# Optimization experiments

Measured on AMD Instinct MI355X. Metric: run time of the kernel, lower is better.

Reference implementation:

```python
import jax, jax.numpy as jnp
import numpy as np

C0 = 32          # cs[0] == cs[1] with planes=[32,32,...], cr=1.0
CIN = 4
EPS = 1e-5

# ---------- host-side coordinate hashing (mirrors F.sphash / F.sphashquery) ----------

def _enc(c):
    # unique int64 code per (x,y,z); +2 shift keeps offset-adjusted coords positive
    return (c[:, 0] + 2).astype(np.int64) + (c[:, 1] + 2).astype(np.int64) * 1024 \
        + (c[:, 2] + 2).astype(np.int64) * 1024 * 1024

def _lookup(sorted_codes, q):
    pos = np.searchsorted(sorted_codes, q)
    pos = np.minimum(pos, len(sorted_codes) - 1)
    return np.where(sorted_codes[pos] == q, pos, -1).astype(np.int32)

def _offsets(r):
    return np.array([[i, j, k] for i in r for j in r for k in r], np.int64)


def setup_inputs() -> dict:
    rng = np.random.default_rng(0)
    N0 = 400000
    pts = rng.integers(0, [400, 400, 40], size=(600000, 3)).astype(np.int64)
    codes = _enc(pts)
    codes_u, idx = np.unique(codes, return_index=True)
    assert len(codes_u) >= N0
    coords0, codes0 = pts[idx][:N0], codes_u[:N0]   # sorted by hash code

    off27, off8 = _offsets([-1, 0, 1]), _offsets([0, 1])
    # ks=3 stride=1 kernel map at level 0: nbr0[k, i] = index of coords0[i]+off27[k] (or -1)
    nbr0 = np.stack([_lookup(codes0, _enc(coords0 + o)) for o in off27])

    # stride-2 downsample coords (level 1)
    c1all = coords0 // 2
    codes1_u, i1 = np.unique(_enc(c1all), return_index=True)
    coords1 = c1all[i1]
    # ks=2 stride=2 kernel map: output voxel gathers inputs at 2*out + {0,1}^3
    down1 = np.stack([_lookup(codes0, _enc(coords1 * 2 + o)) for o in off8])
    # ks=3 stride=1 kernel map at level 1
    nbr1 = np.stack([_lookup(codes1_u, _enc(coords1 + o)) for o in off27])

    key = jax.random.key(0)
    ks = jax.random.split(key, 10)

    def w(k, K, ci, co):
        return jax.random.normal(k, (K, ci, co), jnp.float32) * (1.0 / np.sqrt(K * ci))

    return {
        "voxel_features": jax.random.normal(ks[0], (N0, CIN), jnp.float32),
        "W_stem1": w(ks[1], 27, CIN, C0),
        "W_stem2": w(ks[2], 27, C0, C0),
        "W_down":  w(ks[3], 8,  C0, C0),
        "W_r1a":   w(ks[4], 27, C0, C0),
        "W_r1b":   w(ks[5], 27, C0, C0),
        "W_r2a":   w(ks[6], 27, C0, C0),
        "W_r2b":   w(ks[7], 27, C0, C0),
        "gammas": jnp.ones((7, C0), jnp.float32),
        "betas":  jnp.zeros((7, C0), jnp.float32),
        "nbr0":  jnp.asarray(nbr0),
        "down1": jnp.asarray(down1),
        "nbr1":  jnp.asarray(nbr1),
    }


# ---------- sparse conv: gather-GEMM-scatter per kernel offset ----------

def _spconv(feat, nbr, W):
    # feat [N, Ci], nbr [K, M] (-1 = no neighbor), W [K, Ci, Co] -> out [M, Co]
    def step(acc, kw):
        idx, Wk = kw
        g = jnp.where((idx >= 0)[:, None], feat[jnp.maximum(idx, 0)], 0.0)
        return acc + g @ Wk, None
    acc0 = jnp.zeros((nbr.shape[1], W.shape[-1]), feat.dtype)
    out, _ = jax.lax.scan(step, acc0, (nbr, W))
    return out


def _bn(x, g, b):
    # BatchNorm1d, training-mode statistics (biased var), gamma/beta affine
    mu = x.mean(0)
    var = x.var(0)
    return (x - mu) * jax.lax.rsqrt(var + EPS) * g + b


def _cbr(x, nbr, W, g, b):
    return jax.nn.relu(_bn(_spconv(x, nbr, W), g, b))


def reference(voxel_features, W_stem1, W_stem2, W_down, W_r1a, W_r1b, W_r2a, W_r2b,
              gammas, betas, nbr0, down1, nbr1):
    g, b = gammas, betas
    # stem: two ks=3 sparse convs + BN + ReLU at level 0
    x = _cbr(voxel_features, nbr0, W_stem1, g[0], b[0])
    x = _cbr(x, nbr0, W_stem2, g[1], b[1])
    # stage1: BasicConvolutionBlock (ks=2, stride=2) + 2 ResidualBlocks at level 1
    x1 = _cbr(x, down1, W_down, g[2], b[2])
    h = _cbr(x1, nbr1, W_r1a, g[3], b[3])
    h = _bn(_spconv(h, nbr1, W_r1b), g[4], b[4])
    x1 = jax.nn.relu(h + x1)          # downsample == Identity (inc == outc, stride 1)
    h = _cbr(x1, nbr1, W_r2a, g[5], b[5])
    h = _bn(_spconv(h, nbr1, W_r2b), g[6], b[6])
    return jax.nn.relu(h + x1)
```

## Files before the change

kernel.cpp:

```cpp
#include <hip/hip_runtime.h>

#define EPS 1e-5f

typedef __attribute__((ext_vector_type(8))) short short8;
typedef __attribute__((ext_vector_type(4))) float floatx4;
typedef __attribute__((ext_vector_type(8))) unsigned short ushort8;
typedef __attribute__((ext_vector_type(4))) unsigned short ushortv4;

__device__ __forceinline__ unsigned short f2bf(float f) {
    union { float f; unsigned u; } x; x.f = f;
    unsigned r = x.u + 0x7fffu + ((x.u >> 16) & 1u);
    return (unsigned short)(r >> 16);
}
__device__ __forceinline__ float bf2f(unsigned short b) {
    union { unsigned u; float f; } x; x.u = ((unsigned)b) << 16;
    return x.f;
}

__global__ __launch_bounds__(256) void cvt_kernel(
    const float* __restrict__ x, unsigned short* __restrict__ o, int N)
{
    int t = blockIdx.x * 256 + threadIdx.x;
    if (t >= N) return;
    float4 v = *(const float4*)(x + (size_t)t * 4);
    ushortv4 r = {f2bf(v.x), f2bf(v.y), f2bf(v.z), f2bf(v.w)};
    *(ushortv4*)(o + (size_t)t * 4) = r;
}

__global__ __launch_bounds__(256) void pack_w_kernel(
    const float* __restrict__ W, unsigned short* __restrict__ out, int K)
{
    int t = blockIdx.x * 256 + threadIdx.x;
    if (t >= K * 128) return;
    int lane = t & 63;
    int h = (t >> 6) & 1;
    int k = t >> 7;
    int m = lane & 15, q = lane >> 4;
    ushort8 v;
#pragma unroll
    for (int j = 0; j < 8; ++j)
        v[j] = f2bf(W[((size_t)k * 32 + q * 8 + j) * 32 + h * 16 + m]);
    *(ushort8*)(out + (size_t)t * 8) = v;
}

__global__ __launch_bounds__(256) void pack_w1_kernel(
    const float* __restrict__ W, unsigned short* __restrict__ out)
{
    int t = blockIdx.x * 256 + threadIdx.x;
    if (t >= 512) return;
    int lane = t & 63;
    int h = (t >> 6) & 1;
    int c = t >> 7;
    int m = lane & 15, q = lane >> 4;
    ushort8 v;
#pragma unroll
    for (int j = 0; j < 8; ++j) {
        int kdim = c * 32 + q * 8 + j;
        int tap = kdim >> 2, ci = kdim & 3;
        v[j] = (tap < 27) ? f2bf(W[((size_t)tap * 4 + ci) * 32 + h * 16 + m]) : 0;
    }
    *(ushort8*)(out + (size_t)t * 8) = v;
}

__device__ __forceinline__ void conv_epilogue(
    floatx4 acc00, floatx4 acc01, floatx4 acc10, floatx4 acc11,
    unsigned short* __restrict__ y, float* __restrict__ part,
    int rowbase, int N, float* sm)
{
    const int lane = threadIdx.x & 63;
    const int m = lane & 15, q = lane >> 4;

    if (threadIdx.x < 64) sm[threadIdx.x] = 0.f;
    __syncthreads();

#pragma unroll
    for (int r = 0; r < 4; ++r) {
        int ra = rowbase + q * 4 + r;
        int rb = ra + 16;
        if (ra < N) {
            y[(size_t)ra * 32 + m]      = f2bf(acc00[r]);
            y[(size_t)ra * 32 + 16 + m] = f2bf(acc01[r]);
        }
        if (rb < N) {
            y[(size_t)rb * 32 + m]      = f2bf(acc10[r]);
            y[(size_t)rb * 32 + 16 + m] = f2bf(acc11[r]);
        }
    }

    float s0 = 0.f, q0 = 0.f, s1 = 0.f, q1 = 0.f;
#pragma unroll
    for (int r = 0; r < 4; ++r) {
        s0 += acc00[r] + acc10[r];
        q0 += acc00[r] * acc00[r] + acc10[r] * acc10[r];
        s1 += acc01[r] + acc11[r];
        q1 += acc01[r] * acc01[r] + acc11[r] * acc11[r];
    }
    s0 += __shfl_down(s0, 32); s0 += __shfl_down(s0, 16);
    q0 += __shfl_down(q0, 32); q0 += __shfl_down(q0, 16);
    s1 += __shfl_down(s1, 32); s1 += __shfl_down(s1, 16);
    q1 += __shfl_down(q1, 32); q1 += __shfl_down(q1, 16);
    if (lane < 16) {
        atomicAdd(&sm[m],      s0);
        atomicAdd(&sm[32 + m], q0);
        atomicAdd(&sm[16 + m],      s1);
        atomicAdd(&sm[48 + m], q1);
    }
    __syncthreads();
    if (threadIdx.x < 64)
        part[(size_t)blockIdx.x * 64 + threadIdx.x] = sm[threadIdx.x];
}

template <int K>
__global__ __launch_bounds__(256) void conv_mfma_kernel(
    const unsigned short* __restrict__ x,
    const int* __restrict__ nbr,
    const unsigned short* __restrict__ Wp,
    unsigned short* __restrict__ y,
    float* __restrict__ part, int N)
{
    __shared__ float sm[64];
    const int lane = threadIdx.x & 63;
    const int wave = threadIdx.x >> 6;
    const int m = lane & 15, q = lane >> 4;
    const int rowbase = blockIdx.x * 128 + wave * 32;
    const int row0 = rowbase + m;
    const int row1 = rowbase + 16 + m;

    floatx4 acc00 = {0.f, 0.f, 0.f, 0.f};
    floatx4 acc01 = acc00, acc10 = acc00, acc11 = acc00;

    for (int k = 0; k < K; ++k) {
        int i0 = (row0 < N) ? nbr[(size_t)k * N + row0] : -1;
        int i1 = (row1 < N) ? nbr[(size_t)k * N + row1] : -1;
        short8 a0 = {}, a1 = {};
        if (i0 >= 0) a0 = *(const short8*)(x + (size_t)i0 * 32 + q * 8);
        if (i1 >= 0) a1 = *(const short8*)(x + (size_t)i1 * 32 + q * 8);
        const short8* wk = (const short8*)(Wp + (size_t)k * 2 * 64 * 8);
        short8 b0 = wk[lane];
        short8 b1 = wk[64 + lane];
        acc00 = __builtin_amdgcn_mfma_f32_16x16x32_bf16(a0, b0, acc00, 0, 0, 0);
        acc01 = __builtin_amdgcn_mfma_f32_16x16x32_bf16(a0, b1, acc01, 0, 0, 0);
        acc10 = __builtin_amdgcn_mfma_f32_16x16x32_bf16(a1, b0, acc10, 0, 0, 0);
        acc11 = __builtin_amdgcn_mfma_f32_16x16x32_bf16(a1, b1, acc11, 0, 0, 0);
    }

    conv_epilogue(acc00, acc01, acc10, acc11, y, part, rowbase, N, sm);
}

__global__ __launch_bounds__(256) void conv_stem1_mfma(
    const unsigned short* __restrict__ xb,
    const int* __restrict__ nbr,
    const unsigned short* __restrict__ Wp,
    unsigned short* __restrict__ y,
    float* __restrict__ part, int N)
{
    __shared__ float sm[64];
    const int lane = threadIdx.x & 63;
    const int wave = threadIdx.x >> 6;
    const int m = lane & 15, q = lane >> 4;
    const int rowbase = blockIdx.x * 128 + wave * 32;
    const int row0 = rowbase + m;
    const int row1 = rowbase + 16 + m;

    floatx4 acc00 = {0.f, 0.f, 0.f, 0.f};
    floatx4 acc01 = acc00, acc10 = acc00, acc11 = acc00;

#pragma unroll
    for (int c = 0; c < 4; ++c) {
        const int t0 = c * 8 + q * 2, t1 = t0 + 1;
        short8 a0 = {}, a1 = {};
        {
            int ia = (t0 < 27 && row0 < N) ? nbr[(size_t)t0 * N + row0] : -1;
            int ib = (t1 < 27 && row0 < N) ? nbr[(size_t)t1 * N + row0] : -1;
            ushortv4 ga = {}, gb = {};
            if (ia >= 0) ga = *(const ushortv4*)(xb + (size_t)ia * 4);
            if (ib >= 0) gb = *(const ushortv4*)(xb + (size_t)ib * 4);
            a0[0] = (short)ga[0]; a0[1] = (short)ga[1];
            a0[2] = (short)ga[2]; a0[3] = (short)ga[3];
            a0[4] = (short)gb[0]; a0[5] = (short)gb[1];
            a0[6] = (short)gb[2]; a0[7] = (short)gb[3];
        }
        {
            int ia = (t0 < 27 && row1 < N) ? nbr[(size_t)t0 * N + row1] : -1;
            int ib = (t1 < 27 && row1 < N) ? nbr[(size_t)t1 * N + row1] : -1;
            ushortv4 ga = {}, gb = {};
            if (ia >= 0) ga = *(const ushortv4*)(xb + (size_t)ia * 4);
            if (ib >= 0) gb = *(const ushortv4*)(xb + (size_t)ib * 4);
            a1[0] = (short)ga[0]; a1[1] = (short)ga[1];
            a1[2] = (short)ga[2]; a1[3] = (short)ga[3];
            a1[4] = (short)gb[0]; a1[5] = (short)gb[1];
            a1[6] = (short)gb[2]; a1[7] = (short)gb[3];
        }
        const short8* wk = (const short8*)Wp;
        short8 b0 = wk[(c * 2 + 0) * 64 + lane];
        short8 b1 = wk[(c * 2 + 1) * 64 + lane];
        acc00 = __builtin_amdgcn_mfma_f32_16x16x32_bf16(a0, b0, acc00, 0, 0, 0);
        acc01 = __builtin_amdgcn_mfma_f32_16x16x32_bf16(a0, b1, acc01, 0, 0, 0);
        acc10 = __builtin_amdgcn_mfma_f32_16x16x32_bf16(a1, b0, acc10, 0, 0, 0);
        acc11 = __builtin_amdgcn_mfma_f32_16x16x32_bf16(a1, b1, acc11, 0, 0, 0);
    }

    conv_epilogue(acc00, acc01, acc10, acc11, y, part, rowbase, N, sm);
}

__global__ __launch_bounds__(256) void reduce_stats_kernel(
    const float* __restrict__ part, float* __restrict__ stats, int nb)
{
    __shared__ float sm[256];
    int t = threadIdx.x;
    int c = t & 63, g = t >> 6;
    float s = 0.f;
    for (int b = blockIdx.x * 4 + g; b < nb; b += 256)
        s += part[(size_t)b * 64 + c];
    sm[t] = s;
    __syncthreads();
    if (t < 64)
        atomicAdd(&stats[t], sm[t] + sm[64 + t] + sm[128 + t] + sm[192 + t]);
}

template <bool OUT_F32, bool HAS_RES>
__global__ __launch_bounds__(256) void bn_relu_kernel(
    const unsigned short* __restrict__ y, const float* __restrict__ stats,
    const float* __restrict__ gamma, const float* __restrict__ beta,
    const unsigned short* __restrict__ resid, void* __restrict__ outp, int N)
{
    int t = blockIdx.x * 256 + threadIdx.x;
    if (t >= N) return;
    float inv_n = 1.0f / (float)N;
    const ushort8* yr = (const ushort8*)(y + (size_t)t * 32);

#pragma unroll
    for (int c = 0; c < 4; ++c) {
        ushort8 v = yr[c];
        ushort8 rv = {};
        if (HAS_RES) rv = ((const ushort8*)(resid + (size_t)t * 32))[c];
        float f0, f1, f2, f3, f4, f5, f6, f7;
#define BNJ(fj, j)                                                        \
        {                                                                 \
            int co = c * 8 + (j);                                         \
            float mu = stats[co] * inv_n;                                 \
            float var = stats[32 + co] * inv_n - mu * mu;                 \
            float sc = rsqrtf(var + EPS) * gamma[co];                     \
            fj = (bf2f(v[j]) - mu) * sc + beta[co];                       \
            if (HAS_RES) fj += bf2f(rv[j]);                               \
            fj = fmaxf(fj, 0.0f);                                         \
        }
        BNJ(f0, 0) BNJ(f1, 1) BNJ(f2, 2) BNJ(f3, 3)
        BNJ(f4, 4) BNJ(f5, 5) BNJ(f6, 6) BNJ(f7, 7)
#undef BNJ
        if (OUT_F32) {
            float* ob = (float*)outp + (size_t)t * 32 + c * 8;
            floatx4 u0 = {f0, f1, f2, f3}, u1 = {f4, f5, f6, f7};
            *(floatx4*)(ob) = u0;
            *(floatx4*)(ob + 4) = u1;
        } else {
            ushort8 o;
            o[0] = f2bf(f0); o[1] = f2bf(f1); o[2] = f2bf(f2); o[3] = f2bf(f3);
            o[4] = f2bf(f4); o[5] = f2bf(f5); o[6] = f2bf(f6); o[7] = f2bf(f7);
            ((ushort8*)((unsigned short*)outp + (size_t)t * 32))[c] = o;
        }
    }
}

extern "C" void kernel_launch(void* const* d_in, const int* in_sizes, int n_in,
                              void* d_out, int out_size, void* d_ws, size_t ws_size,
                              hipStream_t stream)
{
    const float* vf   = (const float*)d_in[0];
    const float* Ws1  = (const float*)d_in[1];
    const float* Ws2  = (const float*)d_in[2];
    const float* Wd   = (const float*)d_in[3];
    const float* Wr1a = (const float*)d_in[4];
    const float* Wr1b = (const float*)d_in[5];
    const float* Wr2a = (const float*)d_in[6];
    const float* Wr2b = (const float*)d_in[7];
    const float* gam  = (const float*)d_in[8];
    const float* bet  = (const float*)d_in[9];
    const int* nbr0   = (const int*)d_in[10];
    const int* down1  = (const int*)d_in[11];
    const int* nbr1   = (const int*)d_in[12];

    int N0 = in_sizes[0] / 4;
    int N1 = in_sizes[11] / 8;

    unsigned short* yraw = (unsigned short*)d_ws;
    unsigned short* actA = yraw + (size_t)N0 * 32;
    unsigned short* actB = actA + (size_t)N0 * 32;
    unsigned short* xb   = actB + (size_t)N0 * 32;
    unsigned short* wp   = xb + (size_t)N0 * 4;
    const size_t o_s1  = 0;
    const size_t o_s2  = o_s1 + 4096;
    const size_t o_dn  = o_s2 + 27 * 1024;
    const size_t o_r1a = o_dn + 8 * 1024;
    const size_t o_r1b = o_r1a + 27 * 1024;
    const size_t o_r2a = o_r1b + 27 * 1024;
    const size_t o_r2b = o_r2a + 27 * 1024;
    float* part  = (float*)(wp + o_r2b + 27 * 1024);
    float* stats = part + (size_t)3200 * 64;

    hipMemsetAsync(stats, 0, 7 * 64 * sizeof(float), stream);

    auto g1 = [](int n) { return dim3((unsigned)((n + 255) / 256)); };
    auto gm = [](int n) { return dim3((unsigned)((n + 127) / 128)); };
    int nb0 = (N0 + 127) / 128, nb1 = (N1 + 127) / 128;

    cvt_kernel<<<g1(N0), 256, 0, stream>>>(vf, xb, N0);
    pack_w1_kernel<<<2, 256, 0, stream>>>(Ws1, wp + o_s1);
    pack_w_kernel<<<(27 * 128 + 255) / 256, 256, 0, stream>>>(Ws2,  wp + o_s2,  27);
    pack_w_kernel<<<(8  * 128 + 255) / 256, 256, 0, stream>>>(Wd,   wp + o_dn,  8);
    pack_w_kernel<<<(27 * 128 + 255) / 256, 256, 0, stream>>>(Wr1a, wp + o_r1a, 27);
    pack_w_kernel<<<(27 * 128 + 255) / 256, 256, 0, stream>>>(Wr1b, wp + o_r1b, 27);
    pack_w_kernel<<<(27 * 128 + 255) / 256, 256, 0, stream>>>(Wr2a, wp + o_r2a, 27);
    pack_w_kernel<<<(27 * 128 + 255) / 256, 256, 0, stream>>>(Wr2b, wp + o_r2b, 27);

    conv_stem1_mfma<<<gm(N0), 256, 0, stream>>>(xb, nbr0, wp + o_s1, yraw, part, N0);
    reduce_stats_kernel<<<64, 256, 0, stream>>>(part, stats + 0 * 64, nb0);
    bn_relu_kernel<false, false><<<g1(N0), 256, 0, stream>>>(yraw, stats + 0 * 64, gam + 0, bet + 0, nullptr, actA, N0);
    conv_mfma_kernel<27><<<gm(N0), 256, 0, stream>>>(actA, nbr0, wp + o_s2, yraw, part, N0);
    reduce_stats_kernel<<<64, 256, 0, stream>>>(part, stats + 1 * 64, nb0);
    bn_relu_kernel<false, false><<<g1(N0), 256, 0, stream>>>(yraw, stats + 1 * 64, gam + 32, bet + 32, nullptr, actB, N0);
    conv_mfma_kernel<8><<<gm(N1), 256, 0, stream>>>(actB, down1, wp + o_dn, yraw, part, N1);
    reduce_stats_kernel<<<64, 256, 0, stream>>>(part, stats + 2 * 64, nb1);
    bn_relu_kernel<false, false><<<g1(N1), 256, 0, stream>>>(yraw, stats + 2 * 64, gam + 64, bet + 64, nullptr, actA, N1);
    conv_mfma_kernel<27><<<gm(N1), 256, 0, stream>>>(actA, nbr1, wp + o_r1a, yraw, part, N1);
    reduce_stats_kernel<<<64, 256, 0, stream>>>(part, stats + 3 * 64, nb1);
    bn_relu_kernel<false, false><<<g1(N1), 256, 0, stream>>>(yraw, stats + 3 * 64, gam + 96, bet + 96, nullptr, actB, N1);
    conv_mfma_kernel<27><<<gm(N1), 256, 0, stream>>>(actB, nbr1, wp + o_r1b, yraw, part, N1);
    reduce_stats_kernel<<<64, 256, 0, stream>>>(part, stats + 4 * 64, nb1);
    bn_relu_kernel<false, true><<<g1(N1), 256, 0, stream>>>(yraw, stats + 4 * 64, gam + 128, bet + 128, actA, actB, N1);
    conv_mfma_kernel<27><<<gm(N1), 256, 0, stream>>>(actB, nbr1, wp + o_r2a, yraw, part, N1);
    reduce_stats_kernel<<<64, 256, 0, stream>>>(part, stats + 5 * 64, nb1);
    bn_relu_kernel<false, false><<<g1(N1), 256, 0, stream>>>(yraw, stats + 5 * 64, gam + 160, bet + 160, nullptr, actA, N1);
    conv_mfma_kernel<27><<<gm(N1), 256, 0, stream>>>(actA, nbr1, wp + o_r2b, yraw, part, N1);
    reduce_stats_kernel<<<64, 256, 0, stream>>>(part, stats + 6 * 64, nb1);
    bn_relu_kernel<true, true><<<g1(N1), 256, 0, stream>>>(yraw, stats + 6 * 64, gam + 192, bet + 192, actB, d_out, N1);
}
```

Before: 690.5 us.

## Swizzle conv blocks across XCDs and fuse input/weight prep into one kernel

Conv kernels now remap blockIdx so each of the 8 XCDs processes a contiguous range of row tiles. Because rows are sorted by spatial hash, neighbour gathers from one tile then tend to hit that XCD's own L2. The input conversion and the seven weight-packing kernels are merged into a single prep kernel, cutting seven launches. The partial-stats slot index follows the logical block, so the reduction still sees every tile.

```diff
diff --git a/kernel.cpp b/kernel.cpp
--- a/kernel.cpp
+++ b/kernel.cpp
@@ -7,6 +7,15 @@
 typedef __attribute__((ext_vector_type(8))) unsigned short ushort8;
 typedef __attribute__((ext_vector_type(4))) unsigned short ushortv4;
 
+#define O_S1  0
+#define O_S2  4096
+#define O_DN  (O_S2 + 27648)
+#define O_R1A (O_DN + 8192)
+#define O_R1B (O_R1A + 27648)
+#define O_R2A (O_R1B + 27648)
+#define O_R2B (O_R2A + 27648)
+#define WP_TOTAL (O_R2B + 27648)
+
 __device__ __forceinline__ unsigned short f2bf(float f) {
     union { float f; unsigned u; } x; x.f = f;
     unsigned r = x.u + 0x7fffu + ((x.u >> 16) & 1u);
@@ -17,21 +26,16 @@
     return x.f;
 }
 
-__global__ __launch_bounds__(256) void cvt_kernel(
-    const float* __restrict__ x, unsigned short* __restrict__ o, int N)
-{
-    int t = blockIdx.x * 256 + threadIdx.x;
-    if (t >= N) return;
-    float4 v = *(const float4*)(x + (size_t)t * 4);
-    ushortv4 r = {f2bf(v.x), f2bf(v.y), f2bf(v.z), f2bf(v.w)};
-    *(ushortv4*)(o + (size_t)t * 4) = r;
-}
-
-__global__ __launch_bounds__(256) void pack_w_kernel(
-    const float* __restrict__ W, unsigned short* __restrict__ out, int K)
-{
-    int t = blockIdx.x * 256 + threadIdx.x;
-    if (t >= K * 128) return;
+__device__ __forceinline__ int xcd_swizzle(int nb) {
+    int b = (int)blockIdx.x;
+    int q = nb >> 3, r = nb & 7;
+    int x = b & 7, i = b >> 3;
+    return x * q + (x < r ? x : r) + i;
+}
+
+__device__ __forceinline__ void pack_w_one(
+    const float* __restrict__ W, unsigned short* __restrict__ out, int t)
+{
     int lane = t & 63;
     int h = (t >> 6) & 1;
     int k = t >> 7;
@@ -43,29 +47,55 @@
     *(ushort8*)(out + (size_t)t * 8) = v;
 }
 
-__global__ __launch_bounds__(256) void pack_w1_kernel(
-    const float* __restrict__ W, unsigned short* __restrict__ out)
+__global__ __launch_bounds__(256) void prep_kernel(
+    const float* __restrict__ vf,
+    const float* __restrict__ Ws1, const float* __restrict__ Ws2,
+    const float* __restrict__ Wd,  const float* __restrict__ Wr1a,
+    const float* __restrict__ Wr1b, const float* __restrict__ Wr2a,
+    const float* __restrict__ Wr2b,
+    unsigned short* __restrict__ xb, unsigned short* __restrict__ wp, int N0)
 {
     int t = blockIdx.x * 256 + threadIdx.x;
-    if (t >= 512) return;
-    int lane = t & 63;
-    int h = (t >> 6) & 1;
-    int c = t >> 7;
-    int m = lane & 15, q = lane >> 4;
-    ushort8 v;
-#pragma unroll
-    for (int j = 0; j < 8; ++j) {
-        int kdim = c * 32 + q * 8 + j;
-        int tap = kdim >> 2, ci = kdim & 3;
-        v[j] = (tap < 27) ? f2bf(W[((size_t)tap * 4 + ci) * 32 + h * 16 + m]) : 0;
-    }
-    *(ushort8*)(out + (size_t)t * 8) = v;
+    if (t < N0) {
+        float4 v = *(const float4*)(vf + (size_t)t * 4);
+        ushortv4 r = {f2bf(v.x), f2bf(v.y), f2bf(v.z), f2bf(v.w)};
+        *(ushortv4*)(xb + (size_t)t * 4) = r;
+        return;
+    }
+    t -= N0;
+    if (t < 512) {
+        int lane = t & 63;
+        int h = (t >> 6) & 1;
+        int c = t >> 7;
+        int m = lane & 15, q = lane >> 4;
+        ushort8 v;
+#pragma unroll
+        for (int j = 0; j < 8; ++j) {
+            int kdim = c * 32 + q * 8 + j;
+            int tap = kdim >> 2, ci = kdim & 3;
+            v[j] = (tap < 27) ? f2bf(Ws1[((size_t)tap * 4 + ci) * 32 + h * 16 + m]) : 0;
+        }
+        *(ushort8*)(wp + O_S1 + (size_t)t * 8) = v;
+        return;
+    }
+    t -= 512;
+    if (t < 27 * 128) { pack_w_one(Ws2,  wp + O_S2,  t); return; }
+    t -= 27 * 128;
+    if (t < 8 * 128)  { pack_w_one(Wd,   wp + O_DN,  t); return; }
+    t -= 8 * 128;
+    if (t < 27 * 128) { pack_w_one(Wr1a, wp + O_R1A, t); return; }
+    t -= 27 * 128;
+    if (t < 27 * 128) { pack_w_one(Wr1b, wp + O_R1B, t); return; }
+    t -= 27 * 128;
+    if (t < 27 * 128) { pack_w_one(Wr2a, wp + O_R2A, t); return; }
+    t -= 27 * 128;
+    if (t < 27 * 128) { pack_w_one(Wr2b, wp + O_R2B, t); return; }
 }
 
 __device__ __forceinline__ void conv_epilogue(
     floatx4 acc00, floatx4 acc01, floatx4 acc10, floatx4 acc11,
     unsigned short* __restrict__ y, float* __restrict__ part,
-    int rowbase, int N, float* sm)
+    int rowbase, int lb, int N, float* sm)
 {
     const int lane = threadIdx.x & 63;
     const int m = lane & 15, q = lane >> 4;
@@ -107,7 +137,7 @@
     }
     __syncthreads();
     if (threadIdx.x < 64)
-        part[(size_t)blockIdx.x * 64 + threadIdx.x] = sm[threadIdx.x];
+        part[(size_t)lb * 64 + threadIdx.x] = sm[threadIdx.x];
 }
 
 template <int K>
@@ -119,10 +149,12 @@
     float* __restrict__ part, int N)
 {
     __shared__ float sm[64];
+    const int nb = (N + 127) / 128;
+    const int lb = xcd_swizzle(nb);
     const int lane = threadIdx.x & 63;
     const int wave = threadIdx.x >> 6;
     const int m = lane & 15, q = lane >> 4;
-    const int rowbase = blockIdx.x * 128 + wave * 32;
+    const int rowbase = lb * 128 + wave * 32;
     const int row0 = rowbase + m;
     const int row1 = rowbase + 16 + m;
 
@@ -144,7 +176,7 @@
         acc11 = __builtin_amdgcn_mfma_f32_16x16x32_bf16(a1, b1, acc11, 0, 0, 0);
     }
 
-    conv_epilogue(acc00, acc01, acc10, acc11, y, part, rowbase, N, sm);
+    conv_epilogue(acc00, acc01, acc10, acc11, y, part, rowbase, lb, N, sm);
 }
 
 __global__ __launch_bounds__(256) void conv_stem1_mfma(
@@ -155,10 +187,12 @@
     float* __restrict__ part, int N)
 {
     __shared__ float sm[64];
+    const int nb = (N + 127) / 128;
+    const int lb = xcd_swizzle(nb);
     const int lane = threadIdx.x & 63;
     const int wave = threadIdx.x >> 6;
     const int m = lane & 15, q = lane >> 4;
-    const int rowbase = blockIdx.x * 128 + wave * 32;
+    const int rowbase = lb * 128 + wave * 32;
     const int row0 = rowbase + m;
     const int row1 = rowbase + 16 + m;
 
@@ -200,7 +234,7 @@
         acc11 = __builtin_amdgcn_mfma_f32_16x16x32_bf16(a1, b1, acc11, 0, 0, 0);
     }
 
-    conv_epilogue(acc00, acc01, acc10, acc11, y, part, rowbase, N, sm);
+    conv_epilogue(acc00, acc01, acc10, acc11, y, part, rowbase, lb, N, sm);
 }
 
 __global__ __launch_bounds__(256) void reduce_stats_kernel(
@@ -288,14 +322,7 @@
     unsigned short* actB = actA + (size_t)N0 * 32;
     unsigned short* xb   = actB + (size_t)N0 * 32;
     unsigned short* wp   = xb + (size_t)N0 * 4;
-    const size_t o_s1  = 0;
-    const size_t o_s2  = o_s1 + 4096;
-    const size_t o_dn  = o_s2 + 27 * 1024;
-    const size_t o_r1a = o_dn + 8 * 1024;
-    const size_t o_r1b = o_r1a + 27 * 1024;
-    const size_t o_r2a = o_r1b + 27 * 1024;
-    const size_t o_r2b = o_r2a + 27 * 1024;
-    float* part  = (float*)(wp + o_r2b + 27 * 1024);
+    float* part  = (float*)(wp + WP_TOTAL);
     float* stats = part + (size_t)3200 * 64;
 
     hipMemsetAsync(stats, 0, 7 * 64 * sizeof(float), stream);
@@ -304,34 +331,29 @@
     auto gm = [](int n) { return dim3((unsigned)((n + 127) / 128)); };
     int nb0 = (N0 + 127) / 128, nb1 = (N1 + 127) / 128;
 
-    cvt_kernel<<<g1(N0), 256, 0, stream>>>(vf, xb, N0);
-    pack_w1_kernel<<<2, 256, 0, stream>>>(Ws1, wp + o_s1);
-    pack_w_kernel<<<(27 * 128 + 255) / 256, 256, 0, stream>>>(Ws2,  wp + o_s2,  27);
-    pack_w_kernel<<<(8  * 128 + 255) / 256, 256, 0, stream>>>(Wd,   wp + o_dn,  8);
-    pack_w_kernel<<<(27 * 128 + 255) / 256, 256, 0, stream>>>(Wr1a, wp + o_r1a, 27);
-    pack_w_kernel<<<(27 * 128 + 255) / 256, 256, 0, stream>>>(Wr1b, wp + o_r1b, 27);
-    pack_w_kernel<<<(27 * 128 + 255) / 256, 256, 0, stream>>>(Wr2a, wp + o_r2a, 27);
-    pack_w_kernel<<<(27 * 128 + 255) / 256, 256, 0, stream>>>(Wr2b, wp + o_r2b, 27);
-
-    conv_stem1_mfma<<<gm(N0), 256, 0, stream>>>(xb, nbr0, wp + o_s1, yraw, part, N0);
+    int prep_threads = N0 + 512 + 128 * (27 * 5 + 8);
+    prep_kernel<<<g1(prep_threads), 256, 0, stream>>>(
+        vf, Ws1, Ws2, Wd, Wr1a, Wr1b, Wr2a, Wr2b, xb, wp, N0);
+
+    conv_stem1_mfma<<<gm(N0), 256, 0, stream>>>(xb, nbr0, wp + O_S1, yraw, part, N0);
     reduce_stats_kernel<<<64, 256, 0, stream>>>(part, stats + 0 * 64, nb0);
     bn_relu_kernel<false, false><<<g1(N0), 256, 0, stream>>>(yraw, stats + 0 * 64, gam + 0, bet + 0, nullptr, actA, N0);
-    conv_mfma_kernel<27><<<gm(N0), 256, 0, stream>>>(actA, nbr0, wp + o_s2, yraw, part, N0);
+    conv_mfma_kernel<27><<<gm(N0), 256, 0, stream>>>(actA, nbr0, wp + O_S2, yraw, part, N0);
     reduce_stats_kernel<<<64, 256, 0, stream>>>(part, stats + 1 * 64, nb0);
     bn_relu_kernel<false, false><<<g1(N0), 256, 0, stream>>>(yraw, stats + 1 * 64, gam + 32, bet + 32, nullptr, actB, N0);
-    conv_mfma_kernel<8><<<gm(N1), 256, 0, stream>>>(actB, down1, wp + o_dn, yraw, part, N1);
+    conv_mfma_kernel<8><<<gm(N1), 256, 0, stream>>>(actB, down1, wp + O_DN, yraw, part, N1);
     reduce_stats_kernel<<<64, 256, 0, stream>>>(part, stats + 2 * 64, nb1);
     bn_relu_kernel<false, false><<<g1(N1), 256, 0, stream>>>(yraw, stats + 2 * 64, gam + 64, bet + 64, nullptr, actA, N1);
-    conv_mfma_kernel<27><<<gm(N1), 256, 0, stream>>>(actA, nbr1, wp + o_r1a, yraw, part, N1);
+    conv_mfma_kernel<27><<<gm(N1), 256, 0, stream>>>(actA, nbr1, wp + O_R1A, yraw, part, N1);
     reduce_stats_kernel<<<64, 256, 0, stream>>>(part, stats + 3 * 64, nb1);
     bn_relu_kernel<false, false><<<g1(N1), 256, 0, stream>>>(yraw, stats + 3 * 64, gam + 96, bet + 96, nullptr, actB, N1);
-    conv_mfma_kernel<27><<<gm(N1), 256, 0, stream>>>(actB, nbr1, wp + o_r1b, yraw, part, N1);
+    conv_mfma_kernel<27><<<gm(N1), 256, 0, stream>>>(actB, nbr1, wp + O_R1B, yraw, part, N1);
     reduce_stats_kernel<<<64, 256, 0, stream>>>(part, stats + 4 * 64, nb1);
     bn_relu_kernel<false, true><<<g1(N1), 256, 0, stream>>>(yraw, stats + 4 * 64, gam + 128, bet + 128, actA, actB, N1);
-    conv_mfma_kernel<27><<<gm(N1), 256, 0, stream>>>(actB, nbr1, wp + o_r2a, yraw, part, N1);
+    conv_mfma_kernel<27><<<gm(N1), 256, 0, stream>>>(actB, nbr1, wp + O_R2A, yraw, part, N1);
     reduce_stats_kernel<<<64, 256, 0, stream>>>(part, stats + 5 * 64, nb1);
     bn_relu_kernel<false, false><<<g1(N1), 256, 0, stream>>>(yraw, stats + 5 * 64, gam + 160, bet + 160, nullptr, actA, N1);
-    conv_mfma_kernel<27><<<gm(N1), 256, 0, stream>>>(actA, nbr1, wp + o_r2b, yraw, part, N1);
+    conv_mfma_kernel<27><<<gm(N1), 256, 0, stream>>>(actA, nbr1, wp + O_R2B, yraw, part, N1);
     reduce_stats_kernel<<<64, 256, 0, stream>>>(part, stats + 6 * 64, nb1);
     bn_relu_kernel<true, true><<<g1(N1), 256, 0, stream>>>(yraw, stats + 6 * 64, gam + 192, bet + 192, actB, d_out, N1);
 }
```

After: 632.7 us. -8.4%, faster.
